# Performance work log

Hardware: AMD Instinct MI355X
Metric: run time of the kernel (lower is better)

The kernel has to match this reference:

```python
import jax, jax.numpy as jnp
import numpy as np


def setup_inputs() -> dict:
    key = jax.random.key(0)
    k1, k2 = jax.random.split(key)
    x = jax.random.normal(k1, (32, 64, 64, 64), dtype=jnp.float32)  # [B, C, H, W]
    limit = 3 ** 0.5
    embeddings = jax.random.uniform(k2, (64, 512), dtype=jnp.float32,
                                    minval=-limit, maxval=limit)  # [D, K]
    return {"x": x, "embeddings": embeddings}


def reference(x, embeddings):
    B, D, H, W = x.shape
    # NCHW -> NHWC -> [N, D]
    flat_x = jnp.transpose(x, (0, 2, 3, 1)).reshape(-1, D)
    distances = (
        jnp.sum(flat_x ** 2, axis=1, keepdims=True)
        - 2.0 * flat_x @ embeddings
        + jnp.sum(embeddings ** 2, axis=0, keepdims=True)
    )
    encoding_indices = jnp.argmin(distances, axis=1)  # [N]
    # gather codebook rows: embeddings.T is [K, D]
    quantized = embeddings.T[encoding_indices].reshape(B, H, W, D)
    quantized = jnp.transpose(quantized, (0, 3, 1, 2))  # back to NCHW
    commitment_loss = jnp.mean((x - jax.lax.stop_gradient(quantized)) ** 2)
    # straight-through estimator
    quantized_ste = x + jax.lax.stop_gradient(quantized - x)
    return quantized_ste, commitment_loss, encoding_indices.reshape(B, -1)
```

## Files before the change

### kernel.cpp

```cpp
#include <hip/hip_runtime.h>

#define D      64
#define K      512
#define Q_OFF  0
#define L_OFF  8388608
#define I_OFF  8388609

#define WS_ET    0
#define WS_EN    32768
#define WS_ENH   33280
#define WS_PART  33792
#define WS_BH    40960
#define WS_BL    57344

#define SEL_SCALE 16384.0f
#define SEL_BIAS  (160.0f * 16384.0f)

typedef __attribute__((ext_vector_type(8))) short short8;
typedef __attribute__((ext_vector_type(4))) float f32x4;

static __device__ __forceinline__ unsigned short f2bf(float f) {
    unsigned u = __float_as_uint(f);
    u += 0x7fffu + ((u >> 16) & 1u);
    return (unsigned short)(u >> 16);
}
static __device__ __forceinline__ float bf2f(unsigned short h) {
    return __uint_as_float(((unsigned)h) << 16);
}

__device__ __forceinline__ void gload_lds16(const float* g, float* l) {
    __builtin_amdgcn_global_load_lds(
        (const __attribute__((address_space(1))) unsigned int*)g,
        (__attribute__((address_space(3))) unsigned int*)l, 16, 0, 0);
}

__global__ __launch_bounds__(256) void vq_prep(const float* __restrict__ E,
                                               float* __restrict__ ws) {
    int g = blockIdx.x * 256 + threadIdx.x;
    int t = g >> 6, lane = g & 63;
    int col = lane & 15, kg = lane >> 4;
    int code = t * 16 + col;
    short8* bhp = (short8*)(ws + WS_BH);
    short8* blp = (short8*)(ws + WS_BL);
#pragma unroll
    for (int s = 0; s < 2; ++s) {
        short8 h, l;
#pragma unroll
        for (int j = 0; j < 8; ++j) {
            int k = s * 32 + kg * 8 + j;
            float v = -E[k * K + code];
            unsigned short hb = f2bf(v);
            h[j] = (short)hb;
            l[j] = (short)f2bf(v - bf2f(hb));
        }
        bhp[(t * 2 + s) * 64 + lane] = h;
        blp[(t * 2 + s) * 64 + lane] = l;
    }
    if (g < K) {
        float nsq = 0.f;
#pragma unroll 8
        for (int d = 0; d < D; ++d) {
            float v = E[d * K + g];
            ws[WS_ET + g * D + d] = v;
            nsq = fmaf(v, v, nsq);
        }
        ws[WS_EN + g]  = nsq;
        ws[WS_ENH + g] = 0.5f * nsq;
    }
}

__device__ __forceinline__ float dot16(const float* __restrict__ er,
                                       const float* __restrict__ xv) {
    const float4* e4 = (const float4*)er;
    float a0 = 0.f, a1 = 0.f, a2 = 0.f, a3 = 0.f;
#pragma unroll
    for (int q = 0; q < 4; ++q) {
        float4 e = e4[q];
        a0 = fmaf(xv[4*q+0], e.x, a0);
        a1 = fmaf(xv[4*q+1], e.y, a1);
        a2 = fmaf(xv[4*q+2], e.z, a2);
        a3 = fmaf(xv[4*q+3], e.w, a3);
    }
    return (a0 + a1) + (a2 + a3);
}

__global__ __launch_bounds__(128, 8) void vq_fused(const float* __restrict__ x,
                                                   float* __restrict__ ws,
                                                   float* __restrict__ out,
                                                   float* __restrict__ partial) {
    __shared__ float sbuf[2][1024];
    __shared__ unsigned sc[32];
    __shared__ float2 sdot[4][32];
    __shared__ float wsum2[2];

    const int tid = threadIdx.x, w = tid >> 6, lane = tid & 63;
    const int col = lane & 15, rowg = lane >> 4;
    const int pixw = blockIdx.x * 32 + w * 16;

    const float* bh    = ws + WS_BH;
    const float* bl    = ws + WS_BL;
    const float* enh_g = ws + WS_ENH;

    gload_lds16(bh + tid * 4, sbuf[0] + tid * 4);
    gload_lds16(bl + tid * 4, sbuf[0] + 512 + tid * 4);

    short8 ah[2], al[2];
    {
        int pix = pixw + col;
        const float* xp = x + ((size_t)(pix >> 12) << 18) + (pix & 4095);
#pragma unroll
        for (int s = 0; s < 2; ++s) {
            short8 h, l;
#pragma unroll
            for (int j = 0; j < 8; ++j) {
                float v = xp[(size_t)(s * 32 + rowg * 8 + j) << 12];
                unsigned short hb = f2bf(v);
                h[j] = (short)hb;
                l[j] = (short)f2bf(v - bf2f(hb));
            }
            ah[s] = h; al[s] = l;
        }
    }

    unsigned m1[4], m2[4];
#pragma unroll
    for (int r = 0; r < 4; ++r) { m1[r] = 0xFFFFFFFFu; m2[r] = 0xFFFFFFFFu; }

    __syncthreads();

    for (int c = 0; c < 32; ++c) {
        if (c + 1 < 32) {
            const float* sh = bh + (c + 1) * 512;
            const float* sl = bl + (c + 1) * 512;
            float* db = sbuf[(c + 1) & 1];
            gload_lds16(sh + tid * 4, db + tid * 4);
            gload_lds16(sl + tid * 4, db + 512 + tid * 4);
        }

        const short8* sb = (const short8*)sbuf[c & 1];
        const float ev = enh_g[c * 16 + col];
        const unsigned codev = (unsigned)(c * 16 + col);

        short8 cbh0 = sb[lane];
        short8 cbh1 = sb[64 + lane];
        short8 cbl0 = sb[128 + lane];
        short8 cbl1 = sb[192 + lane];

        f32x4 acc = { ev, ev, ev, ev };
        __builtin_amdgcn_s_setprio(1);
        acc = __builtin_amdgcn_mfma_f32_16x16x32_bf16(ah[0], cbh0, acc, 0, 0, 0);
        acc = __builtin_amdgcn_mfma_f32_16x16x32_bf16(al[0], cbh0, acc, 0, 0, 0);
        acc = __builtin_amdgcn_mfma_f32_16x16x32_bf16(ah[0], cbl0, acc, 0, 0, 0);
        acc = __builtin_amdgcn_mfma_f32_16x16x32_bf16(ah[1], cbh1, acc, 0, 0, 0);
        acc = __builtin_amdgcn_mfma_f32_16x16x32_bf16(al[1], cbh1, acc, 0, 0, 0);
        acc = __builtin_amdgcn_mfma_f32_16x16x32_bf16(ah[1], cbl1, acc, 0, 0, 0);
        __builtin_amdgcn_s_setprio(0);

#pragma unroll
        for (int r = 0; r < 4; ++r) {
            unsigned p0 = (((unsigned)fmaf(acc[r], SEL_SCALE, SEL_BIAS)) << 9) + codev;
            m2[r] = min(m2[r], max(m1[r], p0));
            m1[r] = min(m1[r], p0);
        }

        __syncthreads();
    }

    const int pl   = tid & 31;
    const int part = tid >> 5;
    const int n    = blockIdx.x * 32 + pl;
    const int b    = n >> 12;
    const int hw   = n & 4095;
    const float* xp2 = x + ((size_t)b << 18) + ((size_t)part << 16) + hw;
    float xv2[16];
#pragma unroll
    for (int d = 0; d < 16; ++d) xv2[d] = xp2[(size_t)d << 12];

#pragma unroll
    for (int r = 0; r < 4; ++r) {
        unsigned v1 = m1[r], v2 = m2[r];
#pragma unroll
        for (int m = 1; m < 16; m <<= 1) {
            unsigned o1 = (unsigned)__shfl_xor((int)v1, m, 16);
            unsigned o2 = (unsigned)__shfl_xor((int)v2, m, 16);
            v2 = min(max(v1, o1), min(v2, o2));
            v1 = min(v1, o1);
        }
        if (col == r)
            sc[w * 16 + rowg * 4 + r] = (v1 & 511u) | ((v2 & 511u) << 16);
    }
    __syncthreads();

    const float* ET = ws + WS_ET;
    const float* EN = ws + WS_EN;

    unsigned pk = sc[pl];
    int c1 = (int)(pk & 0xffffu), c2 = (int)(pk >> 16);

    float dp1 = dot16(ET + (c1 << 6) + part * 16, xv2);
    float dp2 = dot16(ET + (c2 << 6) + part * 16, xv2);
    sdot[part][pl] = make_float2(dp1, dp2);
    __syncthreads();
    float2 q0 = sdot[0][pl], q1 = sdot[1][pl], q2 = sdot[2][pl], q3 = sdot[3][pl];
    float d1 = fmaf(-2.f, (q0.x + q1.x) + (q2.x + q3.x), EN[c1]);
    float d2 = fmaf(-2.f, (q0.y + q1.y) + (q2.y + q3.y), EN[c2]);
    bool sw = (d2 < d1) || (d2 == d1 && c2 < c1);
    int bestk = sw ? c2 : c1;

    if (part == 0) out[I_OFF + n] = (float)bestk;

    const float* qv = ET + (bestk << 6) + part * 16;
    float* op = out + Q_OFF + ((size_t)b << 18) + ((size_t)part << 16) + hw;
    float lsum = 0.f;
#pragma unroll
    for (int d = 0; d < 16; ++d) {
        float qd = qv[d];
        op[(size_t)d << 12] = qd;
        float diff = xv2[d] - qd;
        lsum = fmaf(diff, diff, lsum);
    }

#pragma unroll
    for (int off = 32; off > 0; off >>= 1)
        lsum += __shfl_down(lsum, off, 64);
    if ((tid & 63) == 0) wsum2[tid >> 6] = lsum;
    __syncthreads();
    if (tid == 0)
        partial[blockIdx.x] = wsum2[0] + wsum2[1];
}

__global__ __launch_bounds__(256) void vq_final(const float* __restrict__ partial,
                                                float* __restrict__ out) {
    int t = threadIdx.x;
    float s = 0.f;
#pragma unroll
    for (int i = 0; i < 16; ++i) s += partial[t + 256 * i];
#pragma unroll
    for (int off = 32; off > 0; off >>= 1)
        s += __shfl_down(s, off, 64);
    __shared__ float wsum[4];
    if ((t & 63) == 0) wsum[t >> 6] = s;
    __syncthreads();
    if (t == 0)
        out[L_OFF] = ((wsum[0] + wsum[1]) + (wsum[2] + wsum[3])) * (1.f / 8388608.f);
}

extern "C" void kernel_launch(void* const* d_in, const int* in_sizes, int n_in,
                              void* d_out, int out_size, void* d_ws, size_t ws_size,
                              hipStream_t stream) {
    const float* x = (const float*)d_in[0];
    const float* E = (const float*)d_in[1];
    float* out = (float*)d_out;
    float* ws  = (float*)d_ws;

    hipLaunchKernelGGL(vq_prep,  dim3(8),    dim3(256), 0, stream, E, ws);
    hipLaunchKernelGGL(vq_fused, dim3(4096), dim3(128), 0, stream, x, ws, out, ws + WS_PART);
    hipLaunchKernelGGL(vq_final, dim3(1),    dim3(256), 0, stream, ws + WS_PART, out);
}
```

Measured before the change: 66.51 us.

## Drop codebook low-bf16 term and rescore top-4 candidates exactly

The codebook is now stored only as a single bf16 term, which removes the cb_low MFMAs (6 down to 4 per 16-code tile) and halves the codebook bytes streamed into LDS. To make up for the coarser distance, each pixel keeps its top-4 candidates instead of top-2 and rescores all four with exact fp32 dot products. The half-norm bias is computed from the bf16-rounded codebook so it matches what the MFMA sees. In exchange the top-k tracking and shuffle merge use more registers and ALU, and the rescoring gathers twice as many codebook rows.

```diff
diff --git a/kernel.cpp b/kernel.cpp
--- a/kernel.cpp
+++ b/kernel.cpp
@@ -11,7 +11,6 @@
 #define WS_ENH   33280
 #define WS_PART  33792
 #define WS_BH    40960
-#define WS_BL    57344
 
 #define SEL_SCALE 16384.0f
 #define SEL_BIAS  (160.0f * 16384.0f)
@@ -41,31 +40,28 @@
     int col = lane & 15, kg = lane >> 4;
     int code = t * 16 + col;
     short8* bhp = (short8*)(ws + WS_BH);
-    short8* blp = (short8*)(ws + WS_BL);
 #pragma unroll
     for (int s = 0; s < 2; ++s) {
-        short8 h, l;
+        short8 h;
 #pragma unroll
         for (int j = 0; j < 8; ++j) {
             int k = s * 32 + kg * 8 + j;
-            float v = -E[k * K + code];
-            unsigned short hb = f2bf(v);
-            h[j] = (short)hb;
-            l[j] = (short)f2bf(v - bf2f(hb));
+            h[j] = (short)f2bf(-E[k * K + code]);
         }
         bhp[(t * 2 + s) * 64 + lane] = h;
-        blp[(t * 2 + s) * 64 + lane] = l;
     }
     if (g < K) {
-        float nsq = 0.f;
+        float nsq = 0.f, nsqr = 0.f;
 #pragma unroll 8
         for (int d = 0; d < D; ++d) {
             float v = E[d * K + g];
             ws[WS_ET + g * D + d] = v;
             nsq = fmaf(v, v, nsq);
+            float vr = bf2f(f2bf(v));
+            nsqr = fmaf(vr, vr, nsqr);
         }
         ws[WS_EN + g]  = nsq;
-        ws[WS_ENH + g] = 0.5f * nsq;
+        ws[WS_ENH + g] = 0.5f * nsqr;
     }
 }
 
@@ -88,9 +84,8 @@
                                                    float* __restrict__ ws,
                                                    float* __restrict__ out,
                                                    float* __restrict__ partial) {
-    __shared__ float sbuf[2][1024];
-    __shared__ unsigned sc[32];
-    __shared__ float2 sdot[4][32];
+    __shared__ __align__(16) float sbuf[2][1024];
+    __shared__ uint2 sc2[32];
     __shared__ float wsum2[2];
 
     const int tid = threadIdx.x, w = tid >> 6, lane = tid & 63;
@@ -98,11 +93,10 @@
     const int pixw = blockIdx.x * 32 + w * 16;
 
     const float* bh    = ws + WS_BH;
-    const float* bl    = ws + WS_BL;
     const float* enh_g = ws + WS_ENH;
 
-    gload_lds16(bh + tid * 4, sbuf[0] + tid * 4);
-    gload_lds16(bl + tid * 4, sbuf[0] + 512 + tid * 4);
+    gload_lds16(bh + tid * 4,       sbuf[0] + tid * 4);
+    gload_lds16(bh + 512 + tid * 4, sbuf[0] + 512 + tid * 4);
 
     short8 ah[2], al[2];
     {
@@ -122,90 +116,108 @@
         }
     }
 
-    unsigned m1[4], m2[4];
-#pragma unroll
-    for (int r = 0; r < 4; ++r) { m1[r] = 0xFFFFFFFFu; m2[r] = 0xFFFFFFFFu; }
-
-    __syncthreads();
-
-    for (int c = 0; c < 32; ++c) {
-        if (c + 1 < 32) {
-            const float* sh = bh + (c + 1) * 512;
-            const float* sl = bl + (c + 1) * 512;
+    unsigned m1[4], m2[4], m3[4], m4[4];
+#pragma unroll
+    for (int r = 0; r < 4; ++r) { m1[r]=~0u; m2[r]=~0u; m3[r]=~0u; m4[r]=~0u; }
+
+    __syncthreads();
+
+    for (int c = 0; c < 16; ++c) {
+        if (c + 1 < 16) {
+            const float* sh = bh + (c + 1) * 1024;
             float* db = sbuf[(c + 1) & 1];
-            gload_lds16(sh + tid * 4, db + tid * 4);
-            gload_lds16(sl + tid * 4, db + 512 + tid * 4);
+            gload_lds16(sh + tid * 4,       db + tid * 4);
+            gload_lds16(sh + 512 + tid * 4, db + 512 + tid * 4);
         }
 
         const short8* sb = (const short8*)sbuf[c & 1];
-        const float ev = enh_g[c * 16 + col];
-        const unsigned codev = (unsigned)(c * 16 + col);
-
-        short8 cbh0 = sb[lane];
-        short8 cbh1 = sb[64 + lane];
-        short8 cbl0 = sb[128 + lane];
-        short8 cbl1 = sb[192 + lane];
-
-        f32x4 acc = { ev, ev, ev, ev };
-        __builtin_amdgcn_s_setprio(1);
-        acc = __builtin_amdgcn_mfma_f32_16x16x32_bf16(ah[0], cbh0, acc, 0, 0, 0);
-        acc = __builtin_amdgcn_mfma_f32_16x16x32_bf16(al[0], cbh0, acc, 0, 0, 0);
-        acc = __builtin_amdgcn_mfma_f32_16x16x32_bf16(ah[0], cbl0, acc, 0, 0, 0);
-        acc = __builtin_amdgcn_mfma_f32_16x16x32_bf16(ah[1], cbh1, acc, 0, 0, 0);
-        acc = __builtin_amdgcn_mfma_f32_16x16x32_bf16(al[1], cbh1, acc, 0, 0, 0);
-        acc = __builtin_amdgcn_mfma_f32_16x16x32_bf16(ah[1], cbl1, acc, 0, 0, 0);
-        __builtin_amdgcn_s_setprio(0);
-
-#pragma unroll
-        for (int r = 0; r < 4; ++r) {
-            unsigned p0 = (((unsigned)fmaf(acc[r], SEL_SCALE, SEL_BIAS)) << 9) + codev;
-            m2[r] = min(m2[r], max(m1[r], p0));
-            m1[r] = min(m1[r], p0);
-        }
-
+#pragma unroll
+        for (int p = 0; p < 2; ++p) {
+            const int t = c * 2 + p;
+            const float ev = enh_g[t * 16 + col];
+            const unsigned codev = (unsigned)(t * 16 + col);
+
+            short8 cbh0 = sb[p * 128 + lane];
+            short8 cbh1 = sb[p * 128 + 64 + lane];
+
+            f32x4 acc = { ev, ev, ev, ev };
+            __builtin_amdgcn_s_setprio(1);
+            acc = __builtin_amdgcn_mfma_f32_16x16x32_bf16(ah[0], cbh0, acc, 0, 0, 0);
+            acc = __builtin_amdgcn_mfma_f32_16x16x32_bf16(al[0], cbh0, acc, 0, 0, 0);
+            acc = __builtin_amdgcn_mfma_f32_16x16x32_bf16(ah[1], cbh1, acc, 0, 0, 0);
+            acc = __builtin_amdgcn_mfma_f32_16x16x32_bf16(al[1], cbh1, acc, 0, 0, 0);
+            __builtin_amdgcn_s_setprio(0);
+
+#pragma unroll
+            for (int r = 0; r < 4; ++r) {
+                unsigned p0 = (((unsigned)fmaf(acc[r], SEL_SCALE, SEL_BIAS)) << 9) + codev;
+                m4[r] = min(m4[r], max(m3[r], p0));
+                m3[r] = min(m3[r], max(m2[r], p0));
+                m2[r] = min(m2[r], max(m1[r], p0));
+                m1[r] = min(m1[r], p0);
+            }
+        }
         __syncthreads();
     }
 
+#pragma unroll
+    for (int r = 0; r < 4; ++r) {
+        unsigned v1 = m1[r], v2 = m2[r], v3 = m3[r], v4 = m4[r];
+#pragma unroll
+        for (int mm = 1; mm < 16; mm <<= 1) {
+            unsigned o1 = (unsigned)__shfl_xor((int)v1, mm, 16);
+            unsigned o2 = (unsigned)__shfl_xor((int)v2, mm, 16);
+            unsigned o3 = (unsigned)__shfl_xor((int)v3, mm, 16);
+            unsigned o4 = (unsigned)__shfl_xor((int)v4, mm, 16);
+            unsigned z1 = min(v1, o1);
+            unsigned z2 = min(min(v2, o2), max(v1, o1));
+            unsigned z3 = min(min(v3, o3), min(max(v2, o1), max(v1, o2)));
+            unsigned z4 = min(min(min(v4, o4), max(v2, o2)),
+                              min(max(v3, o1), max(v1, o3)));
+            v1 = z1; v2 = z2; v3 = z3; v4 = z4;
+        }
+        if (col == r)
+            sc2[w * 16 + rowg * 4 + r] =
+                make_uint2((v1 & 511u) | ((v2 & 511u) << 16),
+                           (v3 & 511u) | ((v4 & 511u) << 16));
+    }
+    __syncthreads();
+
+    const float* ET = ws + WS_ET;
+    const float* EN = ws + WS_EN;
     const int pl   = tid & 31;
     const int part = tid >> 5;
     const int n    = blockIdx.x * 32 + pl;
     const int b    = n >> 12;
     const int hw   = n & 4095;
+
+    uint2 pk = sc2[pl];
+    int c1 = (int)(pk.x & 0xffffu), c2 = (int)(pk.x >> 16);
+    int c3 = (int)(pk.y & 0xffffu), c4 = (int)(pk.y >> 16);
+
     const float* xp2 = x + ((size_t)b << 18) + ((size_t)part << 16) + hw;
     float xv2[16];
 #pragma unroll
     for (int d = 0; d < 16; ++d) xv2[d] = xp2[(size_t)d << 12];
 
-#pragma unroll
-    for (int r = 0; r < 4; ++r) {
-        unsigned v1 = m1[r], v2 = m2[r];
-#pragma unroll
-        for (int m = 1; m < 16; m <<= 1) {
-            unsigned o1 = (unsigned)__shfl_xor((int)v1, m, 16);
-            unsigned o2 = (unsigned)__shfl_xor((int)v2, m, 16);
-            v2 = min(max(v1, o1), min(v2, o2));
-            v1 = min(v1, o1);
-        }
-        if (col == r)
-            sc[w * 16 + rowg * 4 + r] = (v1 & 511u) | ((v2 & 511u) << 16);
-    }
-    __syncthreads();
-
-    const float* ET = ws + WS_ET;
-    const float* EN = ws + WS_EN;
-
-    unsigned pk = sc[pl];
-    int c1 = (int)(pk & 0xffffu), c2 = (int)(pk >> 16);
-
     float dp1 = dot16(ET + (c1 << 6) + part * 16, xv2);
     float dp2 = dot16(ET + (c2 << 6) + part * 16, xv2);
-    sdot[part][pl] = make_float2(dp1, dp2);
-    __syncthreads();
-    float2 q0 = sdot[0][pl], q1 = sdot[1][pl], q2 = sdot[2][pl], q3 = sdot[3][pl];
+    float dp3 = dot16(ET + (c3 << 6) + part * 16, xv2);
+    float dp4 = dot16(ET + (c4 << 6) + part * 16, xv2);
+    float4* sdot4 = (float4*)&sbuf[0][0];
+    sdot4[part * 32 + pl] = make_float4(dp1, dp2, dp3, dp4);
+    __syncthreads();
+    float4 q0 = sdot4[pl], q1 = sdot4[32 + pl], q2 = sdot4[64 + pl], q3 = sdot4[96 + pl];
     float d1 = fmaf(-2.f, (q0.x + q1.x) + (q2.x + q3.x), EN[c1]);
     float d2 = fmaf(-2.f, (q0.y + q1.y) + (q2.y + q3.y), EN[c2]);
-    bool sw = (d2 < d1) || (d2 == d1 && c2 < c1);
-    int bestk = sw ? c2 : c1;
+    float d3 = fmaf(-2.f, (q0.z + q1.z) + (q2.z + q3.z), EN[c3]);
+    float d4 = fmaf(-2.f, (q0.w + q1.w) + (q2.w + q3.w), EN[c4]);
+
+    float db_ = d1; int cb_ = c1;
+    if (d2 < db_ || (d2 == db_ && c2 < cb_)) { db_ = d2; cb_ = c2; }
+    if (d3 < db_ || (d3 == db_ && c3 < cb_)) { db_ = d3; cb_ = c3; }
+    if (d4 < db_ || (d4 == db_ && c4 < cb_)) { db_ = d4; cb_ = c4; }
+    int bestk = cb_;
 
     if (part == 0) out[I_OFF + n] = (float)bestk;
 
```

Result: slower. 76.36 us (+14.8%).
